# Performance work log

Measured on AMD Instinct MI355X. Metric: run time of the kernel, lower is better.

Reference implementation:

```python
import jax, jax.numpy as jnp
import numpy as np

B, S, D = 2, 2048, 1024
H = 16
HD = D // H
MLP = 4096
EPS = 1e-5


def _layernorm(x, g, b):
    mu = jnp.mean(x, axis=-1, keepdims=True)
    var = jnp.mean(jnp.square(x - mu), axis=-1, keepdims=True)
    return (x - mu) * jax.lax.rsqrt(var + EPS) * g + b


def setup_inputs() -> dict:
    key = jax.random.key(0)
    ks = jax.random.split(key, 16)
    sd = 0.02
    return {
        "x": jax.random.normal(ks[0], (B, S, D), jnp.float32),
        "dis_attn_mask": jax.random.normal(ks[1], (B, S, S), jnp.float32) * 0.1,
        "cls_attn_mask": jax.random.normal(ks[2], (B, S, S), jnp.float32) * 0.1,
        "wq": jax.random.normal(ks[3], (D, D), jnp.float32) * sd,
        "bq": jnp.zeros((D,), jnp.float32),
        "wk": jax.random.normal(ks[4], (D, D), jnp.float32) * sd,
        "bk": jnp.zeros((D,), jnp.float32),
        "wv": jax.random.normal(ks[5], (D, D), jnp.float32) * sd,
        "bv": jnp.zeros((D,), jnp.float32),
        "ln1_g": jnp.ones((D,), jnp.float32),
        "ln1_b": jnp.zeros((D,), jnp.float32),
        "ln2_g": jnp.ones((D,), jnp.float32),
        "ln2_b": jnp.zeros((D,), jnp.float32),
        "w1": jax.random.normal(ks[6], (D, MLP), jnp.float32) * sd,
        "b1": jnp.zeros((MLP,), jnp.float32),
        "w2": jax.random.normal(ks[7], (MLP, D), jnp.float32) * sd,
        "b2": jnp.zeros((D,), jnp.float32),
    }


def reference(x, dis_attn_mask, cls_attn_mask, wq, bq, wk, bk, wv, bv,
              ln1_g, ln1_b, ln2_g, ln2_b, w1, b1, w2, b2):
    res = x
    h = _layernorm(x, ln1_g, ln1_b)
    q = h @ wq + bq
    k = h @ wk + bk
    v = h @ wv + bv
    # NOTE: original torch code uses .view(B, H, S, HD) on a contiguous
    # [B, S, D] tensor (no transpose); row-major reshape reproduces this.
    q = q.reshape(B, H, S, HD)
    k = k.reshape(B, H, S, HD)
    v = v.reshape(B, H, S, HD)
    w = jnp.einsum('bhsd,bhtd->bhst', q, k) * (HD ** -0.5)
    w = w + dis_attn_mask[:, None] + cls_attn_mask[:, None]
    w = jax.nn.softmax(w, axis=-1)
    h_attn = jnp.einsum('bhst,bhtd->bhsd', w, v).reshape(B, S, D)
    h = h_attn + res
    h = _layernorm(h, ln2_g, ln2_b)
    res2 = h
    h = jax.nn.gelu(h @ w1 + b1, approximate=False) @ w2 + b2
    return h + res2
```

## Files before the change

### kernel.cpp

```cpp
#include <hip/hip_runtime.h>
#include <hip/hip_bf16.h>
#include <math.h>

#define BB 2
#define SS 2048
#define DD 1024
#define HH 16
#define MLPD 4096

typedef __attribute__((ext_vector_type(8))) short bf16x8;
typedef __attribute__((ext_vector_type(4))) float f32x4;
typedef __attribute__((ext_vector_type(4))) unsigned short us4;

#define AS1 __attribute__((address_space(1)))
#define AS3 __attribute__((address_space(3)))

static __device__ __forceinline__ void gl_lds16(const void* g, void* l) {
  __builtin_amdgcn_global_load_lds((const AS1 void*)g, (AS3 void*)l, 16, 0, 0);
}

static __device__ __forceinline__ float fast_exp2(float x) {
#if __has_builtin(__builtin_amdgcn_exp2f)
  return __builtin_amdgcn_exp2f(x);
#else
  return exp2f(x);
#endif
}
static __device__ __forceinline__ float fast_rcp(float x) {
#if __has_builtin(__builtin_amdgcn_rcpf)
  return __builtin_amdgcn_rcpf(x);
#else
  return 1.0f / x;
#endif
}

static __device__ __forceinline__ unsigned short f2bf(float f) {
  union { float f; unsigned int u; } v; v.f = f;
  unsigned int r = v.u + 0x7fffu + ((v.u >> 16) & 1u);
  return (unsigned short)(r >> 16);
}
static __device__ __forceinline__ float bf2f(unsigned short b) {
  return __uint_as_float(((unsigned int)b) << 16);
}

static __device__ __forceinline__ float gelu_f(float x) {
  float u = x * x;
  float z = x * fmaf(u, 0.0713548162f, 1.59576912f);
  float e = fast_exp2(z * -1.44269504f);
  return x * fast_rcp(1.0f + e);
}

static __device__ __forceinline__ int swz(int row) {
  return (row & 3) ^ ((row >> 2) & 3);
}

__global__ __launch_bounds__(256) void transpose_to_bf16(
    const float* __restrict__ src, unsigned short* __restrict__ dst,
    int K, int N) {
  __shared__ float tile[32][33];
  int t = threadIdx.x;
  int c = t & 31, rl = t >> 5;
  int bx = blockIdx.x, by = blockIdx.y;
#pragma unroll
  for (int i = 0; i < 4; ++i) {
    int row = rl * 4 + i;
    tile[row][c] = src[(size_t)(by * 32 + row) * N + bx * 32 + c];
  }
  __syncthreads();
#pragma unroll
  for (int i = 0; i < 4; ++i) {
    int n = rl * 4 + i;
    dst[(size_t)(bx * 32 + n) * K + by * 32 + c] = f2bf(tile[c][n]);
  }
}

__global__ __launch_bounds__(256) void transpose_qkv(
    const float* __restrict__ wq, const float* __restrict__ wk,
    const float* __restrict__ wv, unsigned short* __restrict__ dst) {
  __shared__ float tile[32][33];
  const float* src = blockIdx.z == 0 ? wq : blockIdx.z == 1 ? wk : wv;
  unsigned short* d = dst + (size_t)blockIdx.z * 1024 * 1024;
  int t = threadIdx.x;
  int c = t & 31, rl = t >> 5;
  int bx = blockIdx.x, by = blockIdx.y;
#pragma unroll
  for (int i = 0; i < 4; ++i) {
    int row = rl * 4 + i;
    tile[row][c] = src[(size_t)(by * 32 + row) * DD + bx * 32 + c];
  }
  __syncthreads();
#pragma unroll
  for (int i = 0; i < 4; ++i) {
    int n = rl * 4 + i;
    d[(size_t)(bx * 32 + n) * DD + by * 32 + c] = f2bf(tile[c][n]);
  }
}

__global__ __launch_bounds__(256) void concat_bias(
    const float* __restrict__ bq, const float* __restrict__ bk,
    const float* __restrict__ bv, float* __restrict__ dst) {
  int i = blockIdx.x * 256 + threadIdx.x;
  if (i < 1024) dst[i] = bq[i];
  else if (i < 2048) dst[i] = bk[i - 1024];
  else if (i < 3072) dst[i] = bv[i - 2048];
}

__global__ __launch_bounds__(256) void mask_prep(
    const float* __restrict__ dis, const float* __restrict__ cls,
    unsigned short* __restrict__ cm) {
  size_t i = ((size_t)blockIdx.x * 256 + threadIdx.x) * 4;
  float4 d = *(const float4*)(dis + i);
  float4 c = *(const float4*)(cls + i);
  us4 o;
  o[0] = f2bf((d.x + c.x) * 1.44269504f);
  o[1] = f2bf((d.y + c.y) * 1.44269504f);
  o[2] = f2bf((d.z + c.z) * 1.44269504f);
  o[3] = f2bf((d.w + c.w) * 1.44269504f);
  *(us4*)(cm + i) = o;
}

template <bool BF_IN, bool ADD>
__global__ __launch_bounds__(256) void ln_bf16(
    const void* __restrict__ in, const float* __restrict__ add,
    const float* __restrict__ g, const float* __restrict__ beta,
    unsigned short* __restrict__ out) {
  int row = blockIdx.x;
  int t = threadIdx.x;
  float x[4];
  if (BF_IN) {
    us4 b4 = *(const us4*)((const unsigned short*)in + (size_t)row * DD + t * 4);
#pragma unroll
    for (int i = 0; i < 4; ++i) x[i] = bf2f(b4[i]);
  } else {
    float4 f4 = *(const float4*)((const float*)in + (size_t)row * DD + t * 4);
    x[0] = f4.x; x[1] = f4.y; x[2] = f4.z; x[3] = f4.w;
  }
  if (ADD) {
    float4 a4 = *(const float4*)(add + (size_t)row * DD + t * 4);
    x[0] += a4.x; x[1] += a4.y; x[2] += a4.z; x[3] += a4.w;
  }
  float s1 = x[0] + x[1] + x[2] + x[3];
  float s2 = x[0] * x[0] + x[1] * x[1] + x[2] * x[2] + x[3] * x[3];
#pragma unroll
  for (int off = 32; off > 0; off >>= 1) {
    s1 += __shfl_down(s1, off);
    s2 += __shfl_down(s2, off);
  }
  __shared__ float sa[4], sb[4];
  int wid = t >> 6;
  if ((t & 63) == 0) { sa[wid] = s1; sb[wid] = s2; }
  __syncthreads();
  s1 = sa[0] + sa[1] + sa[2] + sa[3];
  s2 = sb[0] + sb[1] + sb[2] + sb[3];
  float mean = s1 * (1.0f / 1024.0f);
  float var = s2 * (1.0f / 1024.0f) - mean * mean;
  float rstd = rsqrtf(var + 1e-5f);
  float4 gv = *(const float4*)(g + t * 4);
  float4 bv = *(const float4*)(beta + t * 4);
  us4 o;
  o[0] = f2bf((x[0] - mean) * rstd * gv.x + bv.x);
  o[1] = f2bf((x[1] - mean) * rstd * gv.y + bv.y);
  o[2] = f2bf((x[2] - mean) * rstd * gv.z + bv.z);
  o[3] = f2bf((x[3] - mean) * rstd * gv.w + bv.w);
  *(us4*)(out + (size_t)row * DD + t * 4) = o;
}

template <int BN, bool GELU, bool ADDSRC, bool OUT_BF16, bool SPLIT3>
__global__ __launch_bounds__(256) void gemm_bf16(
    const unsigned short* __restrict__ A, const unsigned short* __restrict__ BT,
    const float* __restrict__ bias, const unsigned short* __restrict__ addsrc,
    void* C0, void* C1, void* C2, int M, int N, int K) {
  constexpr int BJ = BN / 32;
  __shared__ __align__(16) unsigned short As[2][128][32];
  __shared__ __align__(16) unsigned short Bs[2][BN][32];
  int tid = threadIdx.x;
  int wave = tid >> 6, lane = tid & 63;
  int g = lane >> 4, c16 = lane & 15;
  int m0 = blockIdx.y * 128, n0 = blockIdx.x * BN;
  int wm = (wave >> 1) * 64, wn = (wave & 1) * (BN / 2);
  int lrow = lane >> 2;
  int lsw = (((lane & 3) ^ swz(lrow)) * 8);
  int vA = ((g ^ swz(c16)) * 8);
  const int KI = K / 32;

  {
#pragma unroll
    for (int c = 0; c < 2; ++c) {
      int chunk = wave * 2 + c;
      gl_lds16(A + (size_t)(m0 + chunk * 16 + lrow) * K + lsw, &As[0][chunk * 16][0]);
    }
#pragma unroll
    for (int c = 0; c < BN / 64; ++c) {
      int chunk = wave * (BN / 64) + c;
      gl_lds16(BT + (size_t)(n0 + chunk * 16 + lrow) * K + lsw, &Bs[0][chunk * 16][0]);
    }
  }
  f32x4 acc[4][BJ] = {};
  for (int kt = 0; kt < KI; ++kt) {
    __syncthreads();
    if (kt + 1 < KI) {
      int k0 = (kt + 1) * 32;
      int bn = (kt + 1) & 1;
#pragma unroll
      for (int c = 0; c < 2; ++c) {
        int chunk = wave * 2 + c;
        gl_lds16(A + (size_t)(m0 + chunk * 16 + lrow) * K + k0 + lsw, &As[bn][chunk * 16][0]);
      }
#pragma unroll
      for (int c = 0; c < BN / 64; ++c) {
        int chunk = wave * (BN / 64) + c;
        gl_lds16(BT + (size_t)(n0 + chunk * 16 + lrow) * K + k0 + lsw, &Bs[bn][chunk * 16][0]);
      }
    }
    int buf = kt & 1;
    bf16x8 a[4], b[BJ];
#pragma unroll
    for (int i = 0; i < 4; ++i) a[i] = *(const bf16x8*)&As[buf][wm + i * 16 + c16][vA];
#pragma unroll
    for (int j = 0; j < BJ; ++j) b[j] = *(const bf16x8*)&Bs[buf][wn + j * 16 + c16][vA];
#pragma unroll
    for (int i = 0; i < 4; ++i)
#pragma unroll
      for (int j = 0; j < BJ; ++j)
        acc[i][j] = __builtin_amdgcn_mfma_f32_16x16x32_bf16(a[i], b[j], acc[i][j], 0, 0, 0);
  }
  unsigned short* dstb = nullptr;
  int lc0 = 0;
  if (SPLIT3) {
    int which = n0 >> 10;
    dstb = (unsigned short*)(which == 0 ? C0 : which == 1 ? C1 : C2);
    lc0 = n0 & 1023;
  }
#pragma unroll
  for (int j = 0; j < BJ; ++j) {
    int coff = wn + j * 16 + c16;
    float bj = bias[n0 + coff];
#pragma unroll
    for (int i = 0; i < 4; ++i) {
#pragma unroll
      for (int r = 0; r < 4; ++r) {
        int row = m0 + wm + i * 16 + g * 4 + r;
        float cval = acc[i][j][r] + bj;
        if (GELU) cval = gelu_f(cval);
        if (ADDSRC) cval += bf2f(addsrc[(size_t)row * N + n0 + coff]);
        if (SPLIT3) {
          dstb[(size_t)row * 1024 + lc0 + coff] = f2bf(cval);
        } else if (OUT_BF16) {
          ((unsigned short*)C0)[(size_t)row * N + n0 + coff] = f2bf(cval);
        } else {
          ((float*)C0)[(size_t)row * N + n0 + coff] = cval;
        }
      }
    }
  }
}

__global__ __launch_bounds__(512) void attn_mfma(
    const unsigned short* __restrict__ q, const unsigned short* __restrict__ k,
    const unsigned short* __restrict__ v, const unsigned short* __restrict__ cm,
    unsigned short* __restrict__ outO) {
  __shared__ __align__(16) unsigned short Ks[2][64][32];
  __shared__ __align__(16) unsigned short Vt[64][72];
  __shared__ __align__(16) unsigned short Ps[128][72];
  int tid = threadIdx.x;
  int wave = tid >> 6, lane = tid & 63;
  int g = lane >> 4, c16 = lane & 15;
  int qt = blockIdx.x, h = blockIdx.y, b = blockIdx.z;
  int s0 = qt * 128;
  int wr = wave * 16;
  size_t headoff = (size_t)b * SS * DD + (size_t)h * SS * 64;
  const unsigned short* qb = q + headoff;
  const unsigned short* kb = k + headoff;
  const unsigned short* vb = v + headoff;
  const unsigned short* cmb = cm + (size_t)b * SS * SS;

  int kkey = tid >> 3, kseg = tid & 7;
  unsigned short* kdst = &Ks[kseg >> 2][kkey][((kseg & 3) ^ swz(kkey)) * 8];
  const unsigned short* ksrc = kb + (size_t)kkey * 64 + kseg * 8;
  const unsigned short* vsrc = vb + (size_t)lane * 64 + wave * 8;
  int vK = (g ^ swz(c16)) * 8;

  bf16x8 qf0, qf1;
  {
    size_t qrow = (size_t)(s0 + wr + c16) * 64;
    qf0 = *(const bf16x8*)(qb + qrow);
    qf0 = *(const bf16x8*)(qb + qrow + g * 8);
    qf1 = *(const bf16x8*)(qb + qrow + 32 + g * 8);
  }
  bf16x8 ones;
#pragma unroll
  for (int j = 0; j < 8; ++j) ones[j] = (short)0x3F80;
  f32x4 o[4] = {};
  f32x4 ol = {};
  const float scale2 = 0.18033688f;

  bf16x8 kreg = *(const bf16x8*)(ksrc);
  bf16x8 vreg = *(const bf16x8*)(vsrc);
  unsigned short cmc[4][4];
#pragma unroll
  for (int t = 0; t < 4; ++t)
#pragma unroll
    for (int r = 0; r < 4; ++r)
      cmc[t][r] = cmb[(size_t)(s0 + wr + g * 4 + r) * SS + t * 16 + c16];

  for (int kt = 0; kt < 32; ++kt) {
    __syncthreads();
    *(bf16x8*)kdst = kreg;
#pragma unroll
    for (int j = 0; j < 8; ++j) Vt[wave * 8 + j][lane] = (unsigned short)vreg[j];
    __syncthreads();

    int ktn = kt + 1 < 32 ? kt + 1 : 31;
    bf16x8 kregN = *(const bf16x8*)(ksrc + (size_t)ktn * 4096);
    bf16x8 vregN = *(const bf16x8*)(vsrc + (size_t)ktn * 4096);
    unsigned short cmN[4][4];
#pragma unroll
    for (int t = 0; t < 4; ++t)
#pragma unroll
      for (int r = 0; r < 4; ++r)
        cmN[t][r] = cmb[(size_t)(s0 + wr + g * 4 + r) * SS + ktn * 64 + t * 16 + c16];

    f32x4 s[4] = {};
#pragma unroll
    for (int t = 0; t < 4; ++t) {
      bf16x8 b0 = *(const bf16x8*)&Ks[0][t * 16 + c16][vK];
      bf16x8 b1 = *(const bf16x8*)&Ks[1][t * 16 + c16][vK];
      s[t] = __builtin_amdgcn_mfma_f32_16x16x32_bf16(qf0, b0, s[t], 0, 0, 0);
      s[t] = __builtin_amdgcn_mfma_f32_16x16x32_bf16(qf1, b1, s[t], 0, 0, 0);
    }
#pragma unroll
    for (int t = 0; t < 4; ++t)
#pragma unroll
      for (int r = 0; r < 4; ++r) {
        float p = fast_exp2(fmaf(s[t][r], scale2, bf2f(cmc[t][r])));
        Ps[wr + g * 4 + r][t * 16 + c16] = (unsigned short)(__float_as_uint(p) >> 16);
      }
#pragma unroll
    for (int ks = 0; ks < 2; ++ks) {
      bf16x8 pa = *(const bf16x8*)&Ps[wr + c16][ks * 32 + g * 8];
#pragma unroll
      for (int t2 = 0; t2 < 4; ++t2) {
        bf16x8 vb8 = *(const bf16x8*)&Vt[t2 * 16 + c16][ks * 32 + g * 8];
        o[t2] = __builtin_amdgcn_mfma_f32_16x16x32_bf16(pa, vb8, o[t2], 0, 0, 0);
      }
      ol = __builtin_amdgcn_mfma_f32_16x16x32_bf16(pa, ones, ol, 0, 0, 0);
    }
    kreg = kregN;
    vreg = vregN;
#pragma unroll
    for (int t = 0; t < 4; ++t)
#pragma unroll
      for (int r = 0; r < 4; ++r) cmc[t][r] = cmN[t][r];
  }
  float inv[4];
#pragma unroll
  for (int r = 0; r < 4; ++r) inv[r] = fast_rcp(ol[r]);
#pragma unroll
  for (int t2 = 0; t2 < 4; ++t2)
#pragma unroll
    for (int r = 0; r < 4; ++r) {
      int srow = s0 + wr + g * 4 + r;
      outO[headoff + (size_t)srow * 64 + t2 * 16 + c16] = f2bf(o[t2][r] * inv[r]);
    }
}

extern "C" void kernel_launch(void* const* d_in, const int* in_sizes, int n_in,
                              void* d_out, int out_size, void* d_ws, size_t ws_size,
                              hipStream_t stream) {
  const float* x    = (const float*)d_in[0];
  const float* dis  = (const float*)d_in[1];
  const float* cls  = (const float*)d_in[2];
  const float* wq   = (const float*)d_in[3];
  const float* bq   = (const float*)d_in[4];
  const float* wk   = (const float*)d_in[5];
  const float* bk   = (const float*)d_in[6];
  const float* wv   = (const float*)d_in[7];
  const float* bv   = (const float*)d_in[8];
  const float* ln1g = (const float*)d_in[9];
  const float* ln1b = (const float*)d_in[10];
  const float* ln2g = (const float*)d_in[11];
  const float* ln2b = (const float*)d_in[12];
  const float* w1   = (const float*)d_in[13];
  const float* b1   = (const float*)d_in[14];
  const float* w2   = (const float*)d_in[15];
  const float* b2   = (const float*)d_in[16];
  float* out = (float*)d_out;
  char* ws = (char*)d_ws;

  unsigned short* qkvwT = (unsigned short*)(ws + 0);
  unsigned short* w1T   = (unsigned short*)(ws + 6291456);
  unsigned short* w2T   = (unsigned short*)(ws + 14680064);
  float*          qkvb  = (float*)(ws + 23068672);
  unsigned short* r1    = (unsigned short*)(ws + 23134208);
  unsigned short* qbuf  = (unsigned short*)(ws + 31522816);
  unsigned short* kbuf  = (unsigned short*)(ws + 39911424);
  unsigned short* vbuf  = (unsigned short*)(ws + 48300032);
  unsigned short* h2    = (unsigned short*)(ws + 56688640);
  unsigned short* cmb   = (unsigned short*)(ws + 65077248);
  unsigned short* mm    = (unsigned short*)(ws + 23134208);
  unsigned short* h1 = r1;
  unsigned short* attnO = r1;

  const int rows = BB * SS;

  transpose_qkv<<<dim3(DD / 32, DD / 32, 3), 256, 0, stream>>>(wq, wk, wv, qkvwT);
  transpose_to_bf16<<<dim3(MLPD / 32, DD / 32), 256, 0, stream>>>(w1, w1T, DD, MLPD);
  transpose_to_bf16<<<dim3(DD / 32, MLPD / 32), 256, 0, stream>>>(w2, w2T, MLPD, DD);
  concat_bias<<<12, 256, 0, stream>>>(bq, bk, bv, qkvb);
  mask_prep<<<8192, 256, 0, stream>>>(dis, cls, cmb);

  ln_bf16<false, false><<<rows, 256, 0, stream>>>(x, nullptr, ln1g, ln1b, h1);

  gemm_bf16<128, false, false, true, true><<<dim3(3072 / 128, rows / 128), 256, 0, stream>>>(
      h1, qkvwT, qkvb, nullptr, qbuf, kbuf, vbuf, rows, 3072, DD);

  attn_mfma<<<dim3(SS / 128, HH, BB), 512, 0, stream>>>(qbuf, kbuf, vbuf, cmb, attnO);

  ln_bf16<true, true><<<rows, 256, 0, stream>>>(attnO, x, ln2g, ln2b, h2);

  gemm_bf16<128, true, false, true, false><<<dim3(MLPD / 128, rows / 128), 256, 0, stream>>>(
      h2, w1T, b1, nullptr, mm, nullptr, nullptr, rows, MLPD, DD);

  gemm_bf16<64, false, true, false, false><<<dim3(DD / 64, rows / 128), 256, 0, stream>>>(
      mm, w2T, b2, h2, out, nullptr, nullptr, rows, DD, MLPD);
}
```

Before: 429.7 us.

## Replace direct global-to-LDS loads with register-staged prefetch in GEMM

The GEMM main loop stops using global_load_lds double buffering. It now prefetches two K-tiles ahead into registers and stores them into a single LDS buffer guarded by two barriers per tile. The aim is to hide global latency behind register prefetch depth, at the cost of extra VGPRs, extra barriers and explicit LDS store instructions. A redundant duplicate Q-fragment load in the attention kernel is also removed.

```diff
diff --git a/kernel.cpp b/kernel.cpp
--- a/kernel.cpp
+++ b/kernel.cpp
@@ -11,13 +11,6 @@
 typedef __attribute__((ext_vector_type(8))) short bf16x8;
 typedef __attribute__((ext_vector_type(4))) float f32x4;
 typedef __attribute__((ext_vector_type(4))) unsigned short us4;
-
-#define AS1 __attribute__((address_space(1)))
-#define AS3 __attribute__((address_space(3)))
-
-static __device__ __forceinline__ void gl_lds16(const void* g, void* l) {
-  __builtin_amdgcn_global_load_lds((const AS1 void*)g, (AS3 void*)l, 16, 0, 0);
-}
 
 static __device__ __forceinline__ float fast_exp2(float x) {
 #if __has_builtin(__builtin_amdgcn_exp2f)
@@ -171,58 +164,89 @@
     const float* __restrict__ bias, const unsigned short* __restrict__ addsrc,
     void* C0, void* C1, void* C2, int M, int N, int K) {
   constexpr int BJ = BN / 32;
-  __shared__ __align__(16) unsigned short As[2][128][32];
-  __shared__ __align__(16) unsigned short Bs[2][BN][32];
+  constexpr int BCH = BN / 64;
+  __shared__ __align__(16) unsigned short As[128][32];
+  __shared__ __align__(16) unsigned short Bs[BN][32];
   int tid = threadIdx.x;
   int wave = tid >> 6, lane = tid & 63;
   int g = lane >> 4, c16 = lane & 15;
   int m0 = blockIdx.y * 128, n0 = blockIdx.x * BN;
   int wm = (wave >> 1) * 64, wn = (wave & 1) * (BN / 2);
-  int lrow = lane >> 2;
-  int lsw = (((lane & 3) ^ swz(lrow)) * 8);
-  int vA = ((g ^ swz(c16)) * 8);
+  int lrow = lane >> 2, lq = lane & 3;
+  int dq = (lq ^ swz(lrow)) * 8;
+  const unsigned short* aS = A + (size_t)(m0 + wave * 32 + lrow) * K + lq * 8;
+  unsigned short* aD0 = &As[wave * 32 + lrow][dq];
+  unsigned short* aD1 = &As[wave * 32 + 16 + lrow][dq];
+  const unsigned short* bS = BT + (size_t)(n0 + wave * (BCH * 16) + lrow) * K + lq * 8;
+  unsigned short* bD0 = &Bs[wave * (BCH * 16) + lrow][dq];
+  unsigned short* bD1 = &Bs[(wave * (BCH * 16) + 16 + lrow) % BN][dq];
+  int vA = (g ^ swz(c16)) * 8;
   const int KI = K / 32;
-
-  {
-#pragma unroll
-    for (int c = 0; c < 2; ++c) {
-      int chunk = wave * 2 + c;
-      gl_lds16(A + (size_t)(m0 + chunk * 16 + lrow) * K + lsw, &As[0][chunk * 16][0]);
-    }
-#pragma unroll
-    for (int c = 0; c < BN / 64; ++c) {
-      int chunk = wave * (BN / 64) + c;
-      gl_lds16(BT + (size_t)(n0 + chunk * 16 + lrow) * K + lsw, &Bs[0][chunk * 16][0]);
-    }
-  }
+  const size_t rK = 16 * (size_t)K;
+
+  bf16x8 a0a = *(const bf16x8*)(aS);
+  bf16x8 a1a = *(const bf16x8*)(aS + rK);
+  bf16x8 b0a = *(const bf16x8*)(bS);
+  bf16x8 b1a;
+  if constexpr (BCH == 2) b1a = *(const bf16x8*)(bS + rK);
+  bf16x8 a0b = *(const bf16x8*)(aS + 32);
+  bf16x8 a1b = *(const bf16x8*)(aS + rK + 32);
+  bf16x8 b0b = *(const bf16x8*)(bS + 32);
+  bf16x8 b1b;
+  if constexpr (BCH == 2) b1b = *(const bf16x8*)(bS + rK + 32);
+
   f32x4 acc[4][BJ] = {};
-  for (int kt = 0; kt < KI; ++kt) {
-    __syncthreads();
-    if (kt + 1 < KI) {
-      int k0 = (kt + 1) * 32;
-      int bn = (kt + 1) & 1;
-#pragma unroll
-      for (int c = 0; c < 2; ++c) {
-        int chunk = wave * 2 + c;
-        gl_lds16(A + (size_t)(m0 + chunk * 16 + lrow) * K + k0 + lsw, &As[bn][chunk * 16][0]);
-      }
-#pragma unroll
-      for (int c = 0; c < BN / 64; ++c) {
-        int chunk = wave * (BN / 64) + c;
-        gl_lds16(BT + (size_t)(n0 + chunk * 16 + lrow) * K + k0 + lsw, &Bs[bn][chunk * 16][0]);
-      }
-    }
-    int buf = kt & 1;
-    bf16x8 a[4], b[BJ];
-#pragma unroll
-    for (int i = 0; i < 4; ++i) a[i] = *(const bf16x8*)&As[buf][wm + i * 16 + c16][vA];
-#pragma unroll
-    for (int j = 0; j < BJ; ++j) b[j] = *(const bf16x8*)&Bs[buf][wn + j * 16 + c16][vA];
-#pragma unroll
-    for (int i = 0; i < 4; ++i)
-#pragma unroll
-      for (int j = 0; j < BJ; ++j)
-        acc[i][j] = __builtin_amdgcn_mfma_f32_16x16x32_bf16(a[i], b[j], acc[i][j], 0, 0, 0);
+  for (int kt = 0; kt < KI; kt += 2) {
+    __syncthreads();
+    *(bf16x8*)aD0 = a0a;
+    *(bf16x8*)aD1 = a1a;
+    *(bf16x8*)bD0 = b0a;
+    if constexpr (BCH == 2) *(bf16x8*)bD1 = b1a;
+    __syncthreads();
+    if (kt + 2 < KI) {
+      int ko = (kt + 2) * 32;
+      a0a = *(const bf16x8*)(aS + ko);
+      a1a = *(const bf16x8*)(aS + rK + ko);
+      b0a = *(const bf16x8*)(bS + ko);
+      if constexpr (BCH == 2) b1a = *(const bf16x8*)(bS + rK + ko);
+    }
+    {
+      bf16x8 a[4], b[BJ];
+#pragma unroll
+      for (int i = 0; i < 4; ++i) a[i] = *(const bf16x8*)&As[wm + i * 16 + c16][vA];
+#pragma unroll
+      for (int j = 0; j < BJ; ++j) b[j] = *(const bf16x8*)&Bs[wn + j * 16 + c16][vA];
+#pragma unroll
+      for (int i = 0; i < 4; ++i)
+#pragma unroll
+        for (int j = 0; j < BJ; ++j)
+          acc[i][j] = __builtin_amdgcn_mfma_f32_16x16x32_bf16(a[i], b[j], acc[i][j], 0, 0, 0);
+    }
+    __syncthreads();
+    *(bf16x8*)aD0 = a0b;
+    *(bf16x8*)aD1 = a1b;
+    *(bf16x8*)bD0 = b0b;
+    if constexpr (BCH == 2) *(bf16x8*)bD1 = b1b;
+    __syncthreads();
+    if (kt + 3 < KI) {
+      int ko = (kt + 3) * 32;
+      a0b = *(const bf16x8*)(aS + ko);
+      a1b = *(const bf16x8*)(aS + rK + ko);
+      b0b = *(const bf16x8*)(bS + ko);
+      if constexpr (BCH == 2) b1b = *(const bf16x8*)(bS + rK + ko);
+    }
+    {
+      bf16x8 a[4], b[BJ];
+#pragma unroll
+      for (int i = 0; i < 4; ++i) a[i] = *(const bf16x8*)&As[wm + i * 16 + c16][vA];
+#pragma unroll
+      for (int j = 0; j < BJ; ++j) b[j] = *(const bf16x8*)&Bs[wn + j * 16 + c16][vA];
+#pragma unroll
+      for (int i = 0; i < 4; ++i)
+#pragma unroll
+        for (int j = 0; j < BJ; ++j)
+          acc[i][j] = __builtin_amdgcn_mfma_f32_16x16x32_bf16(a[i], b[j], acc[i][j], 0, 0, 0);
+    }
   }
   unsigned short* dstb = nullptr;
   int lc0 = 0;
@@ -283,7 +307,6 @@
   bf16x8 qf0, qf1;
   {
     size_t qrow = (size_t)(s0 + wr + c16) * 64;
-    qf0 = *(const bf16x8*)(qb + qrow);
     qf0 = *(const bf16x8*)(qb + qrow + g * 8);
     qf1 = *(const bf16x8*)(qb + qrow + 32 + g * 8);
   }
```

Result: faster. 414.0 us (-3.7%).
